# Performance work log

Measured on AMD Instinct MI355X. Metric: run time of the kernel, lower is better.

## Reference

```python
import jax, jax.numpy as jnp
import numpy as np

B, T, D, U = 64, 512, 256, 512


def setup_inputs() -> dict:
    key = jax.random.key(0)
    ks = jax.random.split(key, 8)
    g = lambda k, shape: (jax.random.normal(k, shape, dtype=jnp.float32) * 0.05)
    return {
        "x": jax.random.normal(ks[0], (B, T, D), dtype=jnp.float32),
        "h0": jnp.zeros((B, U), jnp.float32),
        "c0": jnp.zeros((B, U), jnp.float32),
        "W_f_short": g(ks[1], (D + U, U)),
        "b_f_short": -jnp.ones((U,), jnp.float32),
        "W_f_long": g(ks[2], (D + U, U)),
        "b_f_long": jnp.ones((U,), jnp.float32),
        "W_alpha": g(ks[3], (D + U, U)),
        "b_alpha": jnp.zeros((U,), jnp.float32),
        "W_m": g(ks[4], (D + U, D)),
        "b_m": jnp.zeros((D,), jnp.float32),
        "W_C": g(ks[5], (D + U, U)),
        "b_C": jnp.zeros((U,), jnp.float32),
        "W_o": g(ks[6], (D + U, U)),
        "b_o": jnp.zeros((U,), jnp.float32),
    }


def reference(x, h0, c0, W_f_short, b_f_short, W_f_long, b_f_long,
              W_alpha, b_alpha, W_m, b_m, W_C, b_C, W_o, b_o):
    # Fuse the five matmuls that share the same input hx=[h_prev, x_t]
    # into one; W_C uses a different input (hxm) and stays separate.
    units = h0.shape[-1]
    d = x.shape[-1]
    W_cat = jnp.concatenate([W_f_short, W_f_long, W_alpha, W_o, W_m], axis=1)
    b_cat = jnp.concatenate([b_f_short, b_f_long, b_alpha, b_o, b_m], axis=0)
    splits = np.cumsum([units, units, units, units])[:-0 or None]

    def step(carry, x_t):
        h_prev, c_prev = carry
        hx = jnp.concatenate([h_prev, x_t], axis=-1)          # [B, U+D]
        gates = hx @ W_cat + b_cat                            # [B, 4U+D]
        f_short = jax.nn.sigmoid(gates[:, :units])
        f_long = jax.nn.sigmoid(gates[:, units:2 * units])
        alpha = jax.nn.sigmoid(gates[:, 2 * units:3 * units])
        o_t = jax.nn.sigmoid(gates[:, 3 * units:4 * units])
        m_t = jax.nn.sigmoid(gates[:, 4 * units:])            # [B, D]
        f_t = alpha * f_short + (1.0 - alpha) * f_long
        i_t = 1.0 - f_t
        mod_x = m_t * x_t
        hxm = jnp.concatenate([h_prev, mod_x], axis=-1)
        c_hat = jnp.tanh(hxm @ W_C + b_C)
        c_t = f_t * c_prev + i_t * c_hat
        h_t = o_t * jnp.tanh(c_t)
        return (h_t, c_t), h_t

    xs = jnp.swapaxes(x, 0, 1)                                # [T, B, D]
    (_, _), hs = jax.lax.scan(step, (h0, c0), xs)             # hs: [T, B, U]
    return jnp.swapaxes(hs, 0, 1)                             # [B, T, U]
```

## Files before the change

kernel.cpp:

```cpp
#include <hip/hip_runtime.h>
#include <hip/hip_fp16.h>
#include <math.h>

typedef _Float16 h2 __attribute__((ext_vector_type(2)));
typedef _Float16 h8 __attribute__((ext_vector_type(8)));
typedef float    f4 __attribute__((ext_vector_type(4)));
typedef unsigned short     u16;
typedef unsigned int       u32;
typedef unsigned long long u64;

#define BB 64
#define TT 512
#define DD 256
#define UU 512

#define NBLK 64
#define CPB  44
#define XPB  36
#define UPB  8
#define MPB  4
#define NJ   2816
#define NJX  2304

#define OFF_W1   0ull
#define OFF_W2   (OFF_W1 + 2816ull*512*2)
#define OFF_WX   (OFF_W2 + 512ull*256*2)
#define OFF_B1   (OFF_WX + 2304ull*256*2)
#define OFF_HB   (OFF_B1 + 2816ull*4)
#define OFF_MX   (OFF_HB + 64ull*512*2)
#define OFF_CTR  (OFF_MX + 64ull*256*2)
#define OFF_XPRE (OFF_CTR + 16400ull*4)
#define WS_FULL  (OFF_XPRE + 512ull*2304*64*2)

__device__ __forceinline__ float sigf(float v)     { return 1.0f / (1.0f + __expf(-v)); }
__device__ __forceinline__ float tanhfast(float v) { return 1.0f - 2.0f / (__expf(2.0f * v) + 1.0f); }

__device__ __forceinline__ void wait_ctr(u32* c) {
    u32 it = 0;
    while (__hip_atomic_load(c, __ATOMIC_RELAXED, __HIP_MEMORY_SCOPE_AGENT) < (u32)NBLK) {
        __builtin_amdgcn_s_sleep(2);
        if (++it > 4000000u) break;
    }
    (void)__hip_atomic_load(c, __ATOMIC_ACQUIRE, __HIP_MEMORY_SCOPE_AGENT);
}

__device__ __forceinline__ int pk5(int g, int u) { return (u >> 3) * 44 + g * 8 + (u & 7); }
__device__ __forceinline__ int pkm(int d)        { return (d >> 2) * 44 + 40 + (d & 3); }

__global__ void repack_kernel(const float* __restrict__ Wfs, const float* __restrict__ Wfl,
                              const float* __restrict__ Wal, const float* __restrict__ Wm,
                              const float* __restrict__ WC,  const float* __restrict__ Wo,
                              const float* __restrict__ bfs, const float* __restrict__ bfl,
                              const float* __restrict__ bal, const float* __restrict__ bm,
                              const float* __restrict__ bC,  const float* __restrict__ bo,
                              _Float16* __restrict__ W1, _Float16* __restrict__ W2,
                              _Float16* __restrict__ WxT, float* __restrict__ b1,
                              u32* __restrict__ ctr)
{
    const int stride = gridDim.x * blockDim.x;
    const int idx = blockIdx.x * blockDim.x + threadIdx.x;

    for (int i = idx; i < 2816 * 512; i += stride) {
        int J = i >> 9, k = i & 511;
        int blk = J / 44, c = J - blk * 44;
        float v;
        if (c < 40) {
            int grp = c >> 3, u = blk * 8 + (c & 7);
            const float* Wg = (grp == 0) ? Wfs : (grp == 1) ? Wfl : (grp == 2) ? Wal : (grp == 3) ? Wo : WC;
            v = Wg[(size_t)k * 512 + u];
        } else {
            int d = blk * 4 + (c - 40);
            v = Wm[(size_t)k * 256 + d];
        }
        W1[i] = (_Float16)v;
    }
    for (int i = idx; i < 512 * 256; i += stride) {
        int u = i >> 8, dd = i & 255;
        W2[i] = (_Float16)WC[(size_t)(512 + dd) * 512 + u];
    }
    for (int i = idx; i < 2304 * 256; i += stride) {
        int Jx = i >> 8, k2 = i & 255;
        int blk = Jx / 36, lc = Jx - blk * 36;
        float v;
        if (lc < 32) {
            int grp = lc >> 3, u = blk * 8 + (lc & 7);
            const float* Wg = (grp == 0) ? Wfs : (grp == 1) ? Wfl : (grp == 2) ? Wal : Wo;
            v = Wg[(size_t)(512 + k2) * 512 + u];
        } else {
            int d = blk * 4 + (lc - 32);
            v = Wm[(size_t)(512 + k2) * 256 + d];
        }
        WxT[i] = (_Float16)v;
    }
    for (int J = idx; J < 2816; J += stride) {
        int blk = J / 44, c = J - blk * 44;
        float v;
        if (c < 40) {
            int grp = c >> 3, u = blk * 8 + (c & 7);
            v = (grp == 0) ? bfs[u] : (grp == 1) ? bfl[u] : (grp == 2) ? bal[u] : (grp == 3) ? bo[u] : bC[u];
        } else {
            v = bm[blk * 4 + (c - 40)];
        }
        b1[J] = v;
    }
    for (int i = idx; i < 16400; i += stride) ctr[i] = 0;
}

__global__ __launch_bounds__(256) void xpre_kernel(const float* __restrict__ x,
                                                   const _Float16* __restrict__ WxT,
                                                   _Float16* __restrict__ Xpre)
{
    __shared__ _Float16 As[128 * 32];
    __shared__ _Float16 Bs[128 * 32];

    const int tid  = threadIdx.x;
    const int lane = tid & 63;
    const int w    = tid >> 6;
    const int wm   = w >> 1, wn = w & 1;
    const int quad = lane >> 4, l16 = lane & 15;
    const int row0 = blockIdx.x * 128;
    const int n0   = blockIdx.y * 128;

    f4 acc[4][4];
    for (int i = 0; i < 4; ++i)
        for (int j = 0; j < 4; ++j)
            acc[i][j] = (f4){0.f, 0.f, 0.f, 0.f};

    for (int kt = 0; kt < 8; ++kt) {
        const int k0 = kt * 32;
        {
            int r  = tid >> 3;
            int cg = (tid & 7) * 4;
            for (int rr = r; rr < 128; rr += 32) {
                f4 v = *(const f4*)&x[(size_t)(row0 + rr) * 256 + k0 + cg];
                As[rr * 32 + cg + 0] = (_Float16)v.x;
                As[rr * 32 + cg + 1] = (_Float16)v.y;
                As[rr * 32 + cg + 2] = (_Float16)v.z;
                As[rr * 32 + cg + 3] = (_Float16)v.w;
            }
        }
        {
            int r   = tid & 127;
            int seg = (tid >> 7) * 16;
            const _Float16* src = &WxT[(size_t)(n0 + r) * 256 + k0 + seg];
            *(f4*)&Bs[r * 32 + seg]     = *(const f4*)src;
            *(f4*)&Bs[r * 32 + seg + 8] = *(const f4*)(src + 8);
        }
        __syncthreads();

        h8 af[4], bf[4];
#pragma unroll
        for (int f = 0; f < 4; ++f) {
            af[f] = *(const h8*)&As[(wm * 64 + f * 16 + l16) * 32 + quad * 8];
            bf[f] = *(const h8*)&Bs[(wn * 64 + f * 16 + l16) * 32 + quad * 8];
        }
#pragma unroll
        for (int fm = 0; fm < 4; ++fm)
#pragma unroll
            for (int fn = 0; fn < 4; ++fn)
                acc[fm][fn] = __builtin_amdgcn_mfma_f32_16x16x32_f16(af[fm], bf[fn], acc[fm][fn], 0, 0, 0);
        __syncthreads();
    }

#pragma unroll
    for (int fm = 0; fm < 4; ++fm)
#pragma unroll
        for (int fn = 0; fn < 4; ++fn)
#pragma unroll
            for (int r = 0; r < 4; ++r) {
                int rr = row0 + wm * 64 + fm * 16 + quad * 4 + r;
                int J  = n0 + wn * 64 + fn * 16 + l16;
                int b = rr >> 9, tt = rr & 511;
                Xpre[((size_t)tt * NJX + J) * 64 + b] = (_Float16)acc[fm][fn][r];
            }
}

__global__ __launch_bounds__(256, 1) void rnn_coop(
    const float* __restrict__ x, const float* __restrict__ h0, const float* __restrict__ c0,
    const _Float16* __restrict__ W1, const _Float16* __restrict__ W2,
    const float* __restrict__ b1, const _Float16* __restrict__ Xpre,
    _Float16* __restrict__ hbuf, _Float16* __restrict__ mxbuf, u32* __restrict__ ctr,
    float* __restrict__ out)
{
    __shared__ __align__(16) _Float16 sW1[48 * 512];
    __shared__ float sS[48 * 68];
    __shared__ float sF[8 * 64];
    __shared__ float sO[8 * 64];
    __shared__ float sCP[8 * 64];
    __shared__ float sC[8 * 64];
    __shared__ float sB1[44];

    const int tid  = threadIdx.x;
    const int blk  = blockIdx.x;
    const int lane = tid & 63;
    const int w    = tid >> 6;
    const int l16  = lane & 15;
    const int quad = lane >> 4;
    const int swz  = l16 & 7;
    const int br   = w * 16 + l16;

    for (int idx = tid; idx < 48 * 64; idx += 256) {
        int r = idx >> 6, j = idx & 63;
        h8 v = {};
        if (r < CPB) v = *(const h8*)(W1 + ((size_t)(blk * CPB + r) * 512 + j * 8));
        *(h8*)&sW1[(r * 64 + (j ^ (r & 7))) * 8] = v;
    }
    h8 af2[8];
#pragma unroll
    for (int ks = 0; ks < 8; ++ks) {
        af2[ks] = (h8){};
        if (l16 < 8)
            af2[ks] = *(const h8*)(W2 + (size_t)(blk * UPB + l16) * 256 + ks * 32 + quad * 8);
    }
    if (tid < CPB) sB1[tid] = b1[blk * CPB + tid];
    for (int idx = tid; idx < UPB * 64; idx += 256) {
        int u = idx >> 6, b = idx & 63;
        sC[u * 64 + b] = c0[b * UU + blk * UPB + u];
    }
    if (tid < 128) {
        int q = tid >> 6, b = tid & 63;
        _Float16 hp[4];
#pragma unroll
        for (int r = 0; r < 4; ++r) hp[r] = (_Float16)h0[b * UU + blk * UPB + q * 4 + r];
        u64 hq; __builtin_memcpy(&hq, hp, 8);
        __hip_atomic_store((u64*)(hbuf + (size_t)b * 512 + blk * UPB + q * 4), hq,
                           __ATOMIC_RELAXED, __HIP_MEMORY_SCOPE_AGENT);
    }
    __syncthreads();
    if (tid == 0) {
        __hip_atomic_fetch_add(&ctr[1024 * 16], 1u, __ATOMIC_RELAXED, __HIP_MEMORY_SCOPE_AGENT);
        wait_ctr(&ctr[1024 * 16]);
    }
    __syncthreads();

    for (int t = 0; t < TT; ++t) {
        const _Float16* xp = Xpre + ((size_t)t * NJX + blk * XPB) * 64;
        float pfs[2], pfl[2], pal[2], pov[2];
#pragma unroll
        for (int i = 0; i < 2; ++i) {
            int u = w * 2 + i;
            pfs[i] = (float)xp[(size_t)u * 64 + lane];
            pfl[i] = (float)xp[(size_t)(8 + u) * 64 + lane];
            pal[i] = (float)xp[(size_t)(16 + u) * 64 + lane];
            pov[i] = (float)xp[(size_t)(24 + u) * 64 + lane];
        }
        float pxm0 = 0.f, pxm1 = 0.f, pxv0 = 0.f, pxv1 = 0.f;
        int dp = tid >> 6, bm = tid & 63;
        if (tid < 128) {
            pxm0 = (float)xp[(size_t)(32 + 2 * dp) * 64 + bm];
            pxm1 = (float)xp[(size_t)(33 + 2 * dp) * 64 + bm];
            pxv0 = x[((size_t)bm * TT + t) * DD + blk * MPB + 2 * dp];
            pxv1 = x[((size_t)bm * TT + t) * DD + blk * MPB + 2 * dp + 1];
        }

        if (t > 0) {
            if (tid == 0) wait_ctr(&ctr[(2 * (t - 1) + 1) * 16]);
            __syncthreads();
        }

        h8 bf[16];
#pragma unroll
        for (int ks = 0; ks < 16; ++ks)
            bf[ks] = *(const h8*)(hbuf + (size_t)br * 512 + (ks * 4 + quad) * 8);

        f4 acc2 = {0.f, 0.f, 0.f, 0.f};
#pragma unroll
        for (int ks = 0; ks < 16; ++ks) {
            int jx = (ks * 4 + quad) ^ swz;
            h8 a2 = *(const h8*)&sW1[((32 + l16) * 64 + jx) * 8];
            acc2 = __builtin_amdgcn_mfma_f32_16x16x32_f16(a2, bf[ks], acc2, 0, 0, 0);
        }
#pragma unroll
        for (int r = 0; r < 4; ++r)
            sS[(32 + quad * 4 + r) * 68 + br] = acc2[r];
        __syncthreads();

        if (tid < 128) {
            float mr0 = sS[(40 + 2 * dp) * 68 + bm] + sB1[40 + 2 * dp] + pxm0;
            float mr1 = sS[(41 + 2 * dp) * 68 + bm] + sB1[41 + 2 * dp] + pxm1;
            _Float16 m0 = (_Float16)(sigf(mr0) * pxv0);
            _Float16 m1 = (_Float16)(sigf(mr1) * pxv1);
            u16 a, b2; __builtin_memcpy(&a, &m0, 2); __builtin_memcpy(&b2, &m1, 2);
            u32 pk = (u32)a | ((u32)b2 << 16);
            __hip_atomic_store((u32*)(mxbuf + (size_t)bm * 256 + blk * MPB + 2 * dp), pk,
                               __ATOMIC_RELAXED, __HIP_MEMORY_SCOPE_AGENT);
        }
        __syncthreads();
        if (tid == 0)
            __hip_atomic_fetch_add(&ctr[(2 * t) * 16], 1u, __ATOMIC_RELAXED, __HIP_MEMORY_SCOPE_AGENT);

        f4 acc0 = {0.f, 0.f, 0.f, 0.f}, acc1 = {0.f, 0.f, 0.f, 0.f};
#pragma unroll
        for (int ks = 0; ks < 16; ++ks) {
            int jx = (ks * 4 + quad) ^ swz;
            h8 a0 = *(const h8*)&sW1[((     l16) * 64 + jx) * 8];
            h8 a1 = *(const h8*)&sW1[((16 + l16) * 64 + jx) * 8];
            acc0 = __builtin_amdgcn_mfma_f32_16x16x32_f16(a0, bf[ks], acc0, 0, 0, 0);
            acc1 = __builtin_amdgcn_mfma_f32_16x16x32_f16(a1, bf[ks], acc1, 0, 0, 0);
        }
#pragma unroll
        for (int r = 0; r < 4; ++r) {
            sS[(     quad * 4 + r) * 68 + br] = acc0[r];
            sS[(16 + quad * 4 + r) * 68 + br] = acc1[r];
        }
        __syncthreads();

#pragma unroll
        for (int i = 0; i < 2; ++i) {
            int u = w * 2 + i;
            float fs = sigf(sS[u * 68 + lane]        + sB1[u]      + pfs[i]);
            float fl = sigf(sS[(8 + u) * 68 + lane]  + sB1[8 + u]  + pfl[i]);
            float al = sigf(sS[(16 + u) * 68 + lane] + sB1[16 + u] + pal[i]);
            sF[u * 64 + lane]  = al * fs + (1.0f - al) * fl;
            sO[u * 64 + lane]  = sigf(sS[(24 + u) * 68 + lane] + sB1[24 + u] + pov[i]);
            sCP[u * 64 + lane] = sS[(32 + u) * 68 + lane] + sB1[32 + u];
        }
        __syncthreads();

        if (tid == 0) wait_ctr(&ctr[(2 * t) * 16]);
        __syncthreads();

        {
            f4 aq = {0.f, 0.f, 0.f, 0.f};
#pragma unroll
            for (int ks = 0; ks < 8; ++ks) {
                h8 bf2 = *(const h8*)(mxbuf + (size_t)br * 256 + (ks * 4 + quad) * 8);
                aq = __builtin_amdgcn_mfma_f32_16x16x32_f16(af2[ks], bf2, aq, 0, 0, 0);
            }
            if (quad < 2) {
                int u0 = quad * 4;
                float hv[4];
#pragma unroll
                for (int r = 0; r < 4; ++r) {
                    int u = u0 + r;
                    float ch = tanhfast(aq[r] + sCP[u * 64 + br]);
                    float f  = sF[u * 64 + br];
                    float c  = f * sC[u * 64 + br] + (1.0f - f) * ch;
                    sC[u * 64 + br] = c;
                    hv[r] = sO[u * 64 + br] * tanhfast(c);
                }
                _Float16 hp[4] = {(_Float16)hv[0], (_Float16)hv[1], (_Float16)hv[2], (_Float16)hv[3]};
                u64 hq; __builtin_memcpy(&hq, hp, 8);
                __hip_atomic_store((u64*)(hbuf + (size_t)br * 512 + blk * UPB + u0), hq,
                                   __ATOMIC_RELAXED, __HIP_MEMORY_SCOPE_AGENT);
                f4 ovec = {hv[0], hv[1], hv[2], hv[3]};
                __builtin_nontemporal_store(ovec, (f4*)&out[((size_t)br * TT + t) * UU + blk * UPB + u0]);
            }
        }
        __syncthreads();
        if (tid == 0)
            __hip_atomic_fetch_add(&ctr[(2 * t + 1) * 16], 1u, __ATOMIC_RELAXED, __HIP_MEMORY_SCOPE_AGENT);
    }
}

__global__ __launch_bounds__(704) void rnn_fb(const float* __restrict__ x,
                                              const float* __restrict__ h0,
                                              const float* __restrict__ c0,
                                              const _Float16* __restrict__ W1,
                                              const _Float16* __restrict__ W2,
                                              const _Float16* __restrict__ WxT,
                                              const float* __restrict__ b1g,
                                              float* __restrict__ out)
{
    __shared__ float g_ld[2816];
    __shared__ float b1_ld[2816];
    __shared__ float h_ld[512];
    __shared__ float x_ld[256];
    __shared__ float f_ld[512];
    __shared__ float o_ld[512];
    __shared__ float c_ld[512];
    __shared__ __align__(16) h2 hx_h2[256];
    __shared__ __align__(16) h2 x16_h2[128];
    __shared__ __align__(16) h2 modx_h2[128];

    const int tid = threadIdx.x;
    const int b   = blockIdx.x;
    const int j0  = tid * 4;
    const int c   = j0 % 44;
    const bool hasx = (c < 32) || (c >= 40);
    const int Jx0 = (j0 / 44) * 36 + (c < 32 ? c : c - 8);

    for (int j = tid; j < 2816; j += 704) b1_ld[j] = b1g[j];
    if (tid < 512) {
        h_ld[tid] = h0[b * 512 + tid];
        c_ld[tid] = c0[b * 512 + tid];
    }
    __syncthreads();

    const f4* __restrict__ w1r = (const f4*)(W1 + (size_t)j0 * 512);
    const float* __restrict__ xrow = x + (size_t)b * TT * DD;
    float* __restrict__ orow = out + (size_t)b * TT * UU;

    for (int t = 0; t < TT; ++t) {
        if (tid < 256) {
            h2 p; p[0] = (_Float16)h_ld[2 * tid]; p[1] = (_Float16)h_ld[2 * tid + 1];
            hx_h2[tid] = p;
        } else if (tid < 384) {
            int i = tid - 256;
            float v0 = xrow[t * DD + 2 * i];
            float v1 = xrow[t * DD + 2 * i + 1];
            x_ld[2 * i] = v0; x_ld[2 * i + 1] = v1;
            h2 p; p[0] = (_Float16)v0; p[1] = (_Float16)v1;
            x16_h2[i] = p;
        }
        __syncthreads();

        float a0 = b1_ld[j0], a1 = b1_ld[j0 + 1], a2 = b1_ld[j0 + 2], a3 = b1_ld[j0 + 3];
        if (hasx) {
            const f4* xr0 = (const f4*)(WxT + (size_t)Jx0 * 256);
            const f4* xr1 = xr0 + 32;
            const f4* xr2 = xr0 + 64;
            const f4* xr3 = xr0 + 96;
            const f4* xv4 = (const f4*)x16_h2;
#pragma unroll 4
            for (int kc = 0; kc < 32; ++kc) {
                f4 xv = xv4[kc];
                f4 w0 = xr0[kc], w1 = xr1[kc], w2 = xr2[kc], w3 = xr3[kc];
                const h2* xpv = (const h2*)&xv;
                const h2* p0 = (const h2*)&w0; const h2* p1 = (const h2*)&w1;
                const h2* p2 = (const h2*)&w2; const h2* p3 = (const h2*)&w3;
#pragma unroll
                for (int u = 0; u < 4; ++u) {
                    a0 = __builtin_amdgcn_fdot2(p0[u], xpv[u], a0, false);
                    a1 = __builtin_amdgcn_fdot2(p1[u], xpv[u], a1, false);
                    a2 = __builtin_amdgcn_fdot2(p2[u], xpv[u], a2, false);
                    a3 = __builtin_amdgcn_fdot2(p3[u], xpv[u], a3, false);
                }
            }
        }
        {
            const f4* hx4 = (const f4*)hx_h2;
            const f4* r0 = w1r;
            const f4* r1 = w1r + 64;
            const f4* r2 = w1r + 128;
            const f4* r3 = w1r + 192;
#pragma unroll 4
            for (int kc = 0; kc < 64; ++kc) {
                f4 hv = hx4[kc];
                f4 w0 = r0[kc], w1 = r1[kc], w2 = r2[kc], w3 = r3[kc];
                const h2* hp = (const h2*)&hv;
                const h2* p0 = (const h2*)&w0; const h2* p1 = (const h2*)&w1;
                const h2* p2 = (const h2*)&w2; const h2* p3 = (const h2*)&w3;
#pragma unroll
                for (int u = 0; u < 4; ++u) {
                    a0 = __builtin_amdgcn_fdot2(p0[u], hp[u], a0, false);
                    a1 = __builtin_amdgcn_fdot2(p1[u], hp[u], a1, false);
                    a2 = __builtin_amdgcn_fdot2(p2[u], hp[u], a2, false);
                    a3 = __builtin_amdgcn_fdot2(p3[u], hp[u], a3, false);
                }
            }
        }
        g_ld[j0] = a0; g_ld[j0 + 1] = a1; g_ld[j0 + 2] = a2; g_ld[j0 + 3] = a3;
        __syncthreads();

        if (tid < 128) {
            float m0 = sigf(g_ld[pkm(2 * tid)]);
            float m1 = sigf(g_ld[pkm(2 * tid + 1)]);
            h2 p;
            p[0] = (_Float16)(m0 * x_ld[2 * tid]);
            p[1] = (_Float16)(m1 * x_ld[2 * tid + 1]);
            modx_h2[tid] = p;
        } else if (tid < 640) {
            int u = tid - 128;
            float fs = sigf(g_ld[pk5(0, u)]);
            float fl = sigf(g_ld[pk5(1, u)]);
            float al = sigf(g_ld[pk5(2, u)]);
            f_ld[u] = al * fs + (1.0f - al) * fl;
            o_ld[u] = sigf(g_ld[pk5(3, u)]);
        }
        __syncthreads();

        if (tid < 512) {
            float s = g_ld[pk5(4, tid)];
            const f4* w2r = (const f4*)(W2 + (size_t)tid * 256);
            const f4* mx4 = (const f4*)modx_h2;
#pragma unroll 4
            for (int kc = 0; kc < 32; ++kc) {
                f4 wv = w2r[kc];
                f4 mv = mx4[kc];
                const h2* wp = (const h2*)&wv;
                const h2* mp = (const h2*)&mv;
#pragma unroll
                for (int u = 0; u < 4; ++u)
                    s = __builtin_amdgcn_fdot2(wp[u], mp[u], s, false);
            }
            float ch = tanhfast(s);
            float f  = f_ld[tid];
            float cc = f * c_ld[tid] + (1.0f - f) * ch;
            c_ld[tid] = cc;
            float h  = o_ld[tid] * tanhfast(cc);
            h_ld[tid] = h;
            orow[t * UU + tid] = h;
        }
        __syncthreads();
    }
}

extern "C" void kernel_launch(void* const* d_in, const int* in_sizes, int n_in,
                              void* d_out, int out_size, void* d_ws, size_t ws_size,
                              hipStream_t stream)
{
    (void)in_sizes; (void)n_in; (void)out_size;
    const float* x   = (const float*)d_in[0];
    const float* h0  = (const float*)d_in[1];
    const float* c0  = (const float*)d_in[2];
    const float* Wfs = (const float*)d_in[3];
    const float* bfs = (const float*)d_in[4];
    const float* Wfl = (const float*)d_in[5];
    const float* bfl = (const float*)d_in[6];
    const float* Wal = (const float*)d_in[7];
    const float* bal = (const float*)d_in[8];
    const float* Wm  = (const float*)d_in[9];
    const float* bm  = (const float*)d_in[10];
    const float* WC  = (const float*)d_in[11];
    const float* bC  = (const float*)d_in[12];
    const float* Wo  = (const float*)d_in[13];
    const float* bo  = (const float*)d_in[14];

    char* ws = (char*)d_ws;
    _Float16* W1   = (_Float16*)(ws + OFF_W1);
    _Float16* W2   = (_Float16*)(ws + OFF_W2);
    _Float16* WxT  = (_Float16*)(ws + OFF_WX);
    float*    b1   = (float*)   (ws + OFF_B1);
    _Float16* hbuf = (_Float16*)(ws + OFF_HB);
    _Float16* mxbf = (_Float16*)(ws + OFF_MX);
    u32*      ctr  = (u32*)     (ws + OFF_CTR);
    _Float16* Xpre = (_Float16*)(ws + OFF_XPRE);

    repack_kernel<<<dim3(1024), dim3(256), 0, stream>>>(
        Wfs, Wfl, Wal, Wm, WC, Wo, bfs, bfl, bal, bm, bC, bo, W1, W2, WxT, b1, ctr);

    if (ws_size >= WS_FULL) {
        xpre_kernel<<<dim3(256, 18), dim3(256), 0, stream>>>(x, WxT, Xpre);
        rnn_coop<<<dim3(NBLK), dim3(256), 0, stream>>>(
            x, h0, c0, W1, W2, b1, Xpre, hbuf, mxbf, ctr, (float*)d_out);
    } else {
        rnn_fb<<<dim3(BB), dim3(704), 0, stream>>>(
            x, h0, c0, W1, W2, WxT, b1, (float*)d_out);
    }
}
```

Before: 4.397 ms.

## Replace global counter barriers with per-block flags polled by a whole wave

Swaps the shared atomic counters, which every block increments and thread 0 polls, for per-block monotonically increasing flags. A full wave reads all 64 flags in parallel and checks them with a ballot. The m-gate computation now runs straight from the MFMA accumulators in quad 2, which removes an LDS round trip and two block barriers per step. The h-flag is published before the output store so other blocks can proceed sooner. The aim is lower latency on the per-timestep grid barrier, at the cost of relying on correct ordering of the relaxed store plus waitcnt.

```diff
diff --git a/kernel.cpp b/kernel.cpp
--- a/kernel.cpp
+++ b/kernel.cpp
@@ -35,13 +35,15 @@
 __device__ __forceinline__ float sigf(float v)     { return 1.0f / (1.0f + __expf(-v)); }
 __device__ __forceinline__ float tanhfast(float v) { return 1.0f - 2.0f / (__expf(2.0f * v) + 1.0f); }
 
-__device__ __forceinline__ void wait_ctr(u32* c) {
+__device__ __forceinline__ void waitflags_wave(u32* base, u32 tgt, int lane) {
     u32 it = 0;
-    while (__hip_atomic_load(c, __ATOMIC_RELAXED, __HIP_MEMORY_SCOPE_AGENT) < (u32)NBLK) {
-        __builtin_amdgcn_s_sleep(2);
-        if (++it > 4000000u) break;
-    }
-    (void)__hip_atomic_load(c, __ATOMIC_ACQUIRE, __HIP_MEMORY_SCOPE_AGENT);
+    for (;;) {
+        u32 v = __hip_atomic_load(base + lane * 16, __ATOMIC_RELAXED, __HIP_MEMORY_SCOPE_AGENT);
+        if (__ballot(v >= tgt) == ~0ull) break;
+        __builtin_amdgcn_s_sleep(1);
+        if (++it > 2000000u) break;
+    }
+    (void)__hip_atomic_load(base + lane * 16, __ATOMIC_ACQUIRE, __HIP_MEMORY_SCOPE_AGENT);
 }
 
 __device__ __forceinline__ int pk5(int g, int u) { return (u >> 3) * 44 + g * 8 + (u & 7); }
@@ -199,6 +201,9 @@
     const int swz  = l16 & 7;
     const int br   = w * 16 + l16;
 
+    u32* hflag  = ctr;
+    u32* mxflag = ctr + 1024;
+
     for (int idx = tid; idx < 48 * 64; idx += 256) {
         int r = idx >> 6, j = idx & 63;
         h8 v = {};
@@ -227,11 +232,8 @@
                            __ATOMIC_RELAXED, __HIP_MEMORY_SCOPE_AGENT);
     }
     __syncthreads();
-    if (tid == 0) {
-        __hip_atomic_fetch_add(&ctr[1024 * 16], 1u, __ATOMIC_RELAXED, __HIP_MEMORY_SCOPE_AGENT);
-        wait_ctr(&ctr[1024 * 16]);
-    }
-    __syncthreads();
+    if (tid == 0)
+        __hip_atomic_store(&hflag[blk * 16], 1u, __ATOMIC_RELAXED, __HIP_MEMORY_SCOPE_AGENT);
 
     for (int t = 0; t < TT; ++t) {
         const _Float16* xp = Xpre + ((size_t)t * NJX + blk * XPB) * 64;
@@ -244,19 +246,17 @@
             pal[i] = (float)xp[(size_t)(16 + u) * 64 + lane];
             pov[i] = (float)xp[(size_t)(24 + u) * 64 + lane];
         }
-        float pxm0 = 0.f, pxm1 = 0.f, pxv0 = 0.f, pxv1 = 0.f;
-        int dp = tid >> 6, bm = tid & 63;
-        if (tid < 128) {
-            pxm0 = (float)xp[(size_t)(32 + 2 * dp) * 64 + bm];
-            pxm1 = (float)xp[(size_t)(33 + 2 * dp) * 64 + bm];
-            pxv0 = x[((size_t)bm * TT + t) * DD + blk * MPB + 2 * dp];
-            pxv1 = x[((size_t)bm * TT + t) * DD + blk * MPB + 2 * dp + 1];
-        }
-
-        if (t > 0) {
-            if (tid == 0) wait_ctr(&ctr[(2 * (t - 1) + 1) * 16]);
-            __syncthreads();
-        }
+        float pxm[4] = {0.f, 0.f, 0.f, 0.f};
+        f4 pxv = {0.f, 0.f, 0.f, 0.f};
+        if (quad == 2) {
+#pragma unroll
+            for (int r = 0; r < 4; ++r)
+                pxm[r] = (float)xp[(size_t)(32 + r) * 64 + br];
+            pxv = *(const f4*)&x[((size_t)br * TT + t) * DD + blk * MPB];
+        }
+
+        if (w == 0) waitflags_wave(hflag, (u32)(t + 1), lane);
+        __syncthreads();
 
         h8 bf[16];
 #pragma unroll
@@ -270,24 +270,22 @@
             h8 a2 = *(const h8*)&sW1[((32 + l16) * 64 + jx) * 8];
             acc2 = __builtin_amdgcn_mfma_f32_16x16x32_f16(a2, bf[ks], acc2, 0, 0, 0);
         }
-#pragma unroll
-        for (int r = 0; r < 4; ++r)
-            sS[(32 + quad * 4 + r) * 68 + br] = acc2[r];
-        __syncthreads();
-
-        if (tid < 128) {
-            float mr0 = sS[(40 + 2 * dp) * 68 + bm] + sB1[40 + 2 * dp] + pxm0;
-            float mr1 = sS[(41 + 2 * dp) * 68 + bm] + sB1[41 + 2 * dp] + pxm1;
-            _Float16 m0 = (_Float16)(sigf(mr0) * pxv0);
-            _Float16 m1 = (_Float16)(sigf(mr1) * pxv1);
-            u16 a, b2; __builtin_memcpy(&a, &m0, 2); __builtin_memcpy(&b2, &m1, 2);
-            u32 pk = (u32)a | ((u32)b2 << 16);
-            __hip_atomic_store((u32*)(mxbuf + (size_t)bm * 256 + blk * MPB + 2 * dp), pk,
+        if (quad < 2) {
+#pragma unroll
+            for (int r = 0; r < 4; ++r)
+                sS[(32 + quad * 4 + r) * 68 + br] = acc2[r];
+        }
+        if (quad == 2) {
+            _Float16 mp[4];
+#pragma unroll
+            for (int r = 0; r < 4; ++r) {
+                float mr = acc2[r] + sB1[40 + r] + pxm[r];
+                mp[r] = (_Float16)(sigf(mr) * pxv[r]);
+            }
+            u64 mq; __builtin_memcpy(&mq, mp, 8);
+            __hip_atomic_store((u64*)(mxbuf + (size_t)br * 256 + blk * MPB), mq,
                                __ATOMIC_RELAXED, __HIP_MEMORY_SCOPE_AGENT);
         }
-        __syncthreads();
-        if (tid == 0)
-            __hip_atomic_fetch_add(&ctr[(2 * t) * 16], 1u, __ATOMIC_RELAXED, __HIP_MEMORY_SCOPE_AGENT);
 
         f4 acc0 = {0.f, 0.f, 0.f, 0.f}, acc1 = {0.f, 0.f, 0.f, 0.f};
 #pragma unroll
@@ -298,6 +296,9 @@
             acc0 = __builtin_amdgcn_mfma_f32_16x16x32_f16(a0, bf[ks], acc0, 0, 0, 0);
             acc1 = __builtin_amdgcn_mfma_f32_16x16x32_f16(a1, bf[ks], acc1, 0, 0, 0);
         }
+        asm volatile("s_waitcnt vmcnt(0)" ::: "memory");
+        if (quad == 2 && l16 == 0)
+            __hip_atomic_fetch_add(&mxflag[blk * 16], 1u, __ATOMIC_RELAXED, __HIP_MEMORY_SCOPE_AGENT);
 #pragma unroll
         for (int r = 0; r < 4; ++r) {
             sS[(     quad * 4 + r) * 68 + br] = acc0[r];
@@ -317,18 +318,22 @@
         }
         __syncthreads();
 
-        if (tid == 0) wait_ctr(&ctr[(2 * t) * 16]);
+        if (w == 0) waitflags_wave(mxflag, 4u * (u32)(t + 1), lane);
         __syncthreads();
 
         {
+            h8 bf2[8];
+#pragma unroll
+            for (int ks = 0; ks < 8; ++ks)
+                bf2[ks] = *(const h8*)(mxbuf + (size_t)br * 256 + (ks * 4 + quad) * 8);
             f4 aq = {0.f, 0.f, 0.f, 0.f};
 #pragma unroll
-            for (int ks = 0; ks < 8; ++ks) {
-                h8 bf2 = *(const h8*)(mxbuf + (size_t)br * 256 + (ks * 4 + quad) * 8);
-                aq = __builtin_amdgcn_mfma_f32_16x16x32_f16(af2[ks], bf2, aq, 0, 0, 0);
-            }
+            for (int ks = 0; ks < 8; ++ks)
+                aq = __builtin_amdgcn_mfma_f32_16x16x32_f16(af2[ks], bf2[ks], aq, 0, 0, 0);
+
+            f4 ovec = {0.f, 0.f, 0.f, 0.f};
+            const int u0 = quad * 4;
             if (quad < 2) {
-                int u0 = quad * 4;
                 float hv[4];
 #pragma unroll
                 for (int r = 0; r < 4; ++r) {
@@ -343,13 +348,14 @@
                 u64 hq; __builtin_memcpy(&hq, hp, 8);
                 __hip_atomic_store((u64*)(hbuf + (size_t)br * 512 + blk * UPB + u0), hq,
                                    __ATOMIC_RELAXED, __HIP_MEMORY_SCOPE_AGENT);
-                f4 ovec = {hv[0], hv[1], hv[2], hv[3]};
+                ovec = (f4){hv[0], hv[1], hv[2], hv[3]};
+            }
+            __syncthreads();
+            if (tid == 0)
+                __hip_atomic_store(&hflag[blk * 16], (u32)(t + 2), __ATOMIC_RELAXED, __HIP_MEMORY_SCOPE_AGENT);
+            if (quad < 2)
                 __builtin_nontemporal_store(ovec, (f4*)&out[((size_t)br * TT + t) * UU + blk * UPB + u0]);
-            }
-        }
-        __syncthreads();
-        if (tid == 0)
-            __hip_atomic_fetch_add(&ctr[(2 * t + 1) * 16], 1u, __ATOMIC_RELAXED, __HIP_MEMORY_SCOPE_AGENT);
+        }
     }
 }
 
```

After: 4.258 ms. -3.2%, faster.
